# Performance work log

Measured on AMD Instinct MI355X. Metric: run time of the kernel, lower is better.

The kernel has to match this reference:

```python
import jax, jax.numpy as jnp
import numpy as np

LEAKY = 0.1
NSAMPLE = 16


def _gather_group(p, idx):
    # p: [B, N, C], idx: [B, S, K] -> [B, S, K, C]
    return jax.vmap(lambda pb, ib: pb[ib])(p, idx)


def _knn_idx(x, k):
    # x: [B, N, 3]; squared pairwise distances, smallest-k indices
    sq = jnp.sum(x * x, axis=-1)  # [B, N]
    d = sq[:, :, None] + sq[:, None, :] - 2.0 * jnp.einsum('bnc,bmc->bnm', x, x)
    _, idx = jax.lax.top_k(-d, k)  # [B, N, K]
    return idx


def setup_inputs() -> dict:
    key = jax.random.key(0)
    k1, k2, k3, k4, k5 = jax.random.split(key, 5)
    B, N, D = 4, 8192, 32
    m0, m1, m2 = 32, 32, 64
    xyz = jax.random.normal(k1, (B, 3, N), dtype=jnp.float32)
    points = jax.random.normal(k2, (B, D, N), dtype=jnp.float32)
    # Conv2d 1x1 weights (kernel dims squeezed): [out, in]
    W0 = jax.random.normal(k3, (m0, D + 3), dtype=jnp.float32) * (1.0 / np.sqrt(D + 3))
    W1 = jax.random.normal(k4, (m1, m0), dtype=jnp.float32) * (1.0 / np.sqrt(m0))
    W2 = jax.random.normal(k5, (m2, m1), dtype=jnp.float32) * (1.0 / np.sqrt(m1))
    return {'xyz': xyz, 'points': points, 'W0': W0, 'W1': W1, 'W2': W2}


def reference(xyz, points, W0, W1, W2):
    lrelu = lambda x: jax.nn.leaky_relu(x, LEAKY)
    xyz_t = jnp.swapaxes(xyz, 1, 2)  # [B, N, 3]
    # pre-transform point features with feature part of first conv weight
    feat = jnp.einsum('oc,bcn->bno', W0[:, 3:], points)  # [B, N, m0]
    idx = _knn_idx(xyz_t, NSAMPLE)  # [B, N, K]
    grouped_xyz = _gather_group(xyz_t, idx)              # [B, N, K, 3]
    grouped_norm = grouped_xyz - xyz_t[:, :, None, :]    # relative coords
    grouped_feat = _gather_group(feat, idx)              # [B, N, K, m0]
    # first conv: xyz-part applied to relative coords + already-transformed feats
    x = jnp.einsum('oc,bnkc->bonk', W0[:, :3], grouped_norm) \
        + jnp.transpose(grouped_feat, (0, 3, 1, 2))      # [B, m0, N, K]
    x = lrelu(x)
    x = lrelu(jnp.einsum('oc,bcnk->bonk', W1, x))        # [B, m1, N, K]
    x = lrelu(jnp.einsum('oc,bcnk->bonk', W2, x))        # [B, m2, N, K]
    return jnp.max(x, axis=-1)                           # [B, m2, N]
```

## Files before the change

kernel.cpp:

```cpp
#include <hip/hip_runtime.h>

#define NP   8192
#define BB   4
#define DIN  32
#define M0   32
#define M1   32
#define M2   64
#define CAP  80
#define CSTR 81
#define KQ   32

typedef float f32x2 __attribute__((ext_vector_type(2)));
typedef float f32x4 __attribute__((ext_vector_type(4)));
typedef short bf16x8 __attribute__((ext_vector_type(8)));

__device__ __forceinline__ float lrelu(float x) { return fmaxf(x, 0.1f * x); }
__device__ __forceinline__ unsigned umin_(unsigned a, unsigned b) { return a < b ? a : b; }
__device__ __forceinline__ unsigned umax_(unsigned a, unsigned b) { return a > b ? a : b; }

__device__ __forceinline__ unsigned fkey(float f) {
    unsigned b = __float_as_uint(f);
    return (b & 0x80000000u) ? ~b : (b | 0x80000000u);
}
__device__ __forceinline__ float funkey(unsigned k) {
    unsigned b = (k & 0x80000000u) ? (k & 0x7fffffffu) : ~k;
    return __uint_as_float(b);
}

__device__ __forceinline__ unsigned bf16rn(float f) {
    unsigned u = __float_as_uint(f);
    unsigned r = (u >> 16) & 1u;
    return (u + 0x7fffu + r) >> 16;
}

__device__ __forceinline__ f32x2 pk_fma(f32x2 a, f32x2 b, f32x2 c) {
    f32x2 d;
    asm("v_pk_fma_f32 %0, %1, %2, %3" : "=v"(d) : "v"(a), "s"(b), "v"(c));
    return d;
}

__device__ __forceinline__ void split_pack2(float f0, float f1, unsigned& hp, unsigned& lp) {
    unsigned u0 = __float_as_uint(f0), u1 = __float_as_uint(f1);
    unsigned h0 = u0 & 0xffff0000u, h1 = u1 & 0xffff0000u;
    hp = (u0 >> 16) | h1;
    float r0 = f0 - __uint_as_float(h0);
    float r1 = f1 - __uint_as_float(h1);
    lp = (__float_as_uint(r0) >> 16) | (__float_as_uint(r1) & 0xffff0000u);
}

__device__ __forceinline__ void wfrag(const float* wrow, bf16x8& h, bf16x8& lo) {
    float4 a = *(const float4*)(wrow);
    float4 b = *(const float4*)(wrow + 4);
    unsigned* hv = (unsigned*)&h;
    unsigned* lv = (unsigned*)&lo;
    split_pack2(a.x, a.y, hv[0], lv[0]);
    split_pack2(a.z, a.w, hv[1], lv[1]);
    split_pack2(b.x, b.y, hv[2], lv[2]);
    split_pack2(b.z, b.w, hv[3], lv[3]);
}

__device__ __forceinline__ f32x4 mfma16(bf16x8 a, bf16x8 b, f32x4 c) {
    return __builtin_amdgcn_mfma_f32_16x16x32_bf16(a, b, c, 0, 0, 0);
}

__global__ __launch_bounds__(256) void prep_kernel(
    const float* __restrict__ xyz, const float* __restrict__ points,
    const float* __restrict__ W0, const float* __restrict__ W1,
    const float* __restrict__ W2, float4* __restrict__ pts4,
    float4* __restrict__ ptsS, unsigned* __restrict__ featb,
    uint4* __restrict__ w1f, uint4* __restrict__ w2f)
{
    const int tid  = threadIdx.x;
    const int w    = __builtin_amdgcn_readfirstlane(tid >> 6);
    const int lane = tid & 63;
    const int t    = blockIdx.x * 64 + lane;
    const int b    = t >> 13;
    const int n    = t & (NP - 1);

    if (w == 0) {
        const float* xb = xyz + (size_t)b * 3 * NP;
        float x = xb[n], y = xb[NP + n], z = xb[2 * NP + n];
        float s = x * x + y * y + z * z;
        pts4[t] = make_float4(x, y, z, s);
        ptsS[t] = make_float4(-2.f * x, -2.f * y, -2.f * z, s);
    }

    const float* pb = points + (size_t)b * DIN * NP + n;
    float p[DIN];
#pragma unroll
    for (int c = 0; c < DIN; ++c) p[c] = pb[c * NP];

    uint4 outv;
    unsigned* ov = (unsigned*)&outv;
#pragma unroll
    for (int r = 0; r < 4; ++r) {
        int oe = w * 8 + 2 * r;
        float a0 = 0.f, a1 = 0.f;
#pragma unroll
        for (int c = 0; c < DIN; ++c) {
            a0 = fmaf(W0[oe * 35 + 3 + c], p[c], a0);
            a1 = fmaf(W0[(oe + 1) * 35 + 3 + c], p[c], a1);
        }
        ov[r] = bf16rn(a0) | (bf16rn(a1) << 16);
    }
    *(uint4*)(featb + (size_t)t * 16 + w * 4) = outv;

    if (blockIdx.x == 0 && tid < 64) {
        const int qq = tid & 15, gg = tid >> 4;
        bf16x8 h, lo;
#pragma unroll
        for (int r = 0; r < 2; ++r) {
            wfrag(W1 + (16 * r + qq) * 32 + gg * 8, h, lo);
            w1f[(r * 64 + tid) * 2 + 0] = *(uint4*)&h;
            w1f[(r * 64 + tid) * 2 + 1] = *(uint4*)&lo;
        }
#pragma unroll
        for (int rr = 0; rr < 4; ++rr) {
            wfrag(W2 + (16 * rr + qq) * 32 + gg * 8, h, lo);
            w2f[(rr * 64 + tid) * 2 + 0] = *(uint4*)&h;
            w2f[(rr * 64 + tid) * 2 + 1] = *(uint4*)&lo;
        }
    }
}

__global__ __launch_bounds__(512, 8) void knn_kernel(const float4* __restrict__ pts4,
                                                     const float4* __restrict__ ptsS,
                                                     int* __restrict__ idxout)
{
    __shared__ unsigned skey[KQ * 65];
    __shared__ float    sT[KQ];
    __shared__ int      scnt[KQ];
    __shared__ float    cand_t[KQ * CSTR];
    __shared__ int      cand_i[KQ * CSTR];

    const int tid  = threadIdx.x;
    const int w    = __builtin_amdgcn_readfirstlane(tid >> 6);
    const int lane = tid & 63;
    const int blk  = blockIdx.x;
    const int b    = blk >> 8;
    const int n0   = (blk & 255) << 5;
    const int bn0  = b * NP;
    const float4* P  = pts4 + bn0;
    const float4* S  = ptsS + bn0;
    const float4* Pq = P + n0;

    for (int i = tid; i < KQ * 65; i += 512) skey[i] = 0xFFFFFFFFu;
    if (tid < KQ) scnt[tid] = 0;
    __syncthreads();

    const int base = w * 1024;

#pragma unroll 1
    for (int sg = 0; sg < 2; ++sg) {
        const int sb = base + sg * 512;
        f32x2 sx[4], sy[4], sz[4], sw2[4];
#pragma unroll
        for (int jp = 0; jp < 4; ++jp) {
            float4 a = S[sb + (2 * jp) * 64 + lane];
            float4 c = S[sb + (2 * jp + 1) * 64 + lane];
            sx[jp].x = a.x;  sx[jp].y = c.x;
            sy[jp].x = a.y;  sy[jp].y = c.y;
            sz[jp].x = a.z;  sz[jp].y = c.z;
            sw2[jp].x = a.w; sw2[jp].y = c.w;
        }
#pragma unroll 1
        for (int qc = 0; qc < 4; ++qc) {
            float4 qv[8];
#pragma unroll
            for (int i = 0; i < 8; ++i) qv[i] = Pq[qc * 8 + i];
#pragma unroll
            for (int i = 0; i < 8; ++i) {
                f32x2 qx, qy, qz;
                qx.x = qv[i].x; qx.y = qv[i].x;
                qy.x = qv[i].y; qy.y = qv[i].y;
                qz.x = qv[i].z; qz.y = qv[i].z;
                f32x2 t0 = pk_fma(sz[0], qz, sw2[0]);
                f32x2 t1 = pk_fma(sz[1], qz, sw2[1]);
                f32x2 t2 = pk_fma(sz[2], qz, sw2[2]);
                f32x2 t3 = pk_fma(sz[3], qz, sw2[3]);
                t0 = pk_fma(sy[0], qy, t0);  t1 = pk_fma(sy[1], qy, t1);
                t2 = pk_fma(sy[2], qy, t2);  t3 = pk_fma(sy[3], qy, t3);
                t0 = pk_fma(sx[0], qx, t0);  t1 = pk_fma(sx[1], qx, t1);
                t2 = pk_fma(sx[2], qx, t2);  t3 = pk_fma(sx[3], qx, t3);
                float a  = fminf(fminf(t0.x, t0.y), t1.x);
                float b2 = fminf(fminf(t1.y, t2.x), t2.y);
                float c2 = fminf(fminf(t3.x, t3.y), a);
                float mn = fminf(b2, c2);
                atomicMin(&skey[(qc * 8 + i) * 65 + lane], fkey(mn));
            }
        }
    }
    __syncthreads();

    if (tid < KQ) {
        unsigned t16[16];
#pragma unroll
        for (int i = 0; i < 16; ++i) t16[i] = 0xFFFFFFFFu;
        for (int c = 0; c < 64; ++c) {
            unsigned d = skey[tid * 65 + c];
            if (d < t16[15]) {
                t16[15] = d;
#pragma unroll
                for (int i = 15; i > 0; --i) {
                    unsigned a = t16[i - 1], cc = t16[i];
                    t16[i - 1] = umin_(a, cc);
                    t16[i]     = umax_(a, cc);
                }
            }
        }
        sT[tid] = funkey(t16[15]);
    }
    __syncthreads();

#pragma unroll 1
    for (int sg = 0; sg < 2; ++sg) {
        const int sb = base + sg * 512;
        f32x2 sx[4], sy[4], sz[4], sw2[4];
#pragma unroll
        for (int jp = 0; jp < 4; ++jp) {
            float4 a = S[sb + (2 * jp) * 64 + lane];
            float4 c = S[sb + (2 * jp + 1) * 64 + lane];
            sx[jp].x = a.x;  sx[jp].y = c.x;
            sy[jp].x = a.y;  sy[jp].y = c.y;
            sz[jp].x = a.z;  sz[jp].y = c.z;
            sw2[jp].x = a.w; sw2[jp].y = c.w;
        }
#pragma unroll 1
        for (int qc = 0; qc < 4; ++qc) {
            float4 qv[8];
#pragma unroll
            for (int i = 0; i < 8; ++i) qv[i] = Pq[qc * 8 + i];
#pragma unroll
            for (int i = 0; i < 8; ++i) {
                const int q = qc * 8 + i;
                const float T = sT[q];
                f32x2 qx, qy, qz;
                qx.x = qv[i].x; qx.y = qv[i].x;
                qy.x = qv[i].y; qy.y = qv[i].y;
                qz.x = qv[i].z; qz.y = qv[i].z;
#pragma unroll
                for (int jp = 0; jp < 4; ++jp) {
                    f32x2 t = pk_fma(sz[jp], qz, sw2[jp]);
                    t = pk_fma(sy[jp], qy, t);
                    t = pk_fma(sx[jp], qx, t);
                    if (t.x <= T) {
                        int pos = atomicAdd(&scnt[q], 1);
                        if (pos < CAP) {
                            cand_t[q * CSTR + pos] = t.x;
                            cand_i[q * CSTR + pos] = sb + (2 * jp) * 64 + lane;
                        }
                    }
                    if (t.y <= T) {
                        int pos = atomicAdd(&scnt[q], 1);
                        if (pos < CAP) {
                            cand_t[q * CSTR + pos] = t.y;
                            cand_i[q * CSTR + pos] = sb + (2 * jp + 1) * 64 + lane;
                        }
                    }
                }
            }
        }
    }
    __syncthreads();

    if (tid < KQ) {
        int cnt = scnt[tid];
        int* outp = idxout + ((bn0 + n0 + tid) << 4);
        float bd[16]; int bi[16];
#pragma unroll
        for (int i = 0; i < 16; ++i) { bd[i] = 3e38f; bi[i] = 0; }
        if (cnt <= CAP) {
            for (int pos = 0; pos < cnt; ++pos) {
                float d = cand_t[tid * CSTR + pos];
                int   j = cand_i[tid * CSTR + pos];
                if ((d < bd[15]) || (d == bd[15] && j < bi[15])) {
                    bd[15] = d; bi[15] = j;
#pragma unroll
                    for (int i = 15; i > 0; --i) {
                        bool sw = (bd[i] < bd[i - 1]) || (bd[i] == bd[i - 1] && bi[i] < bi[i - 1]);
                        float td = bd[i - 1]; int tj = bi[i - 1];
                        bd[i - 1] = sw ? bd[i] : td;  bi[i - 1] = sw ? bi[i] : tj;
                        bd[i]     = sw ? td : bd[i];  bi[i]     = sw ? tj : bi[i];
                    }
                }
            }
        } else {
            float4 q4 = Pq[tid];
            for (int j = 0; j < NP; ++j) {
                float4 s = S[j];
                float d = fmaf(q4.x, s.x, fmaf(q4.y, s.y, fmaf(q4.z, s.z, s.w)));
                if ((d < bd[15]) || (d == bd[15] && j < bi[15])) {
                    bd[15] = d; bi[15] = j;
#pragma unroll
                    for (int i = 15; i > 0; --i) {
                        bool sw = (bd[i] < bd[i - 1]) || (bd[i] == bd[i - 1] && bi[i] < bi[i - 1]);
                        float td = bd[i - 1]; int tj = bi[i - 1];
                        bd[i - 1] = sw ? bd[i] : td;  bi[i - 1] = sw ? bi[i] : tj;
                        bd[i]     = sw ? td : bd[i];  bi[i]     = sw ? tj : bi[i];
                    }
                }
            }
        }
#pragma unroll
        for (int i = 0; i < 16; ++i) outp[i] = bi[i];
    }
}

__global__ __launch_bounds__(256, 4) void conv_kernel(
    const float4* __restrict__ pts4, const unsigned* __restrict__ featb,
    const int* __restrict__ idx, const float* __restrict__ W0,
    const uint4* __restrict__ w1f, const uint4* __restrict__ w2f,
    float* __restrict__ out)
{
    __shared__ __align__(16) unsigned short sh_hi[4][4][64][8];
    __shared__ __align__(16) unsigned short sh_lo[4][4][64][8];
    __shared__ float so[M2][17];

    const int tid = threadIdx.x;
    const int w   = __builtin_amdgcn_readfirstlane(tid >> 6);
    const int l   = tid & 63;
    const int g   = l >> 4;
    const int q   = l & 15;
    const int k   = tid & 15;
    const int nl  = tid >> 4;
    const int blk = blockIdx.x;
    const int b   = blk >> 9;
    const int n0  = (blk & 511) << 4;
    const int n   = n0 + nl;
    const int bn  = b * NP + n;
    const int j   = idx[(bn << 4) + k];
    const int bj  = b * NP + j;

    const float4 pc = pts4[bn];
    const float4 pj = pts4[bj];
    const float rx = pj.x - pc.x, ry = pj.y - pc.y, rz = pj.z - pc.z;

    const uint4* fj = (const uint4*)(featb + (size_t)bj * 16);

#pragma unroll
    for (int gg = 0; gg < 4; ++gg) {
        uint4 u = fj[gg];
        const unsigned* uv = (const unsigned*)&u;
        uint4 hv, lv;
        unsigned* hp = (unsigned*)&hv;
        unsigned* lp = (unsigned*)&lv;
#pragma unroll
        for (int r = 0; r < 4; ++r) {
            int o = gg * 8 + 2 * r;
            float fe  = __uint_as_float(uv[r] << 16);
            float fo_ = __uint_as_float(uv[r] & 0xffff0000u);
            float e0 = lrelu(fmaf(W0[o * 35], rx, fmaf(W0[o * 35 + 1], ry, fmaf(W0[o * 35 + 2], rz, fe))));
            float e1 = lrelu(fmaf(W0[(o + 1) * 35], rx, fmaf(W0[(o + 1) * 35 + 1], ry, fmaf(W0[(o + 1) * 35 + 2], rz, fo_))));
            split_pack2(e0, e1, hp[r], lp[r]);
        }
        *(uint4*)&sh_hi[w][gg][l][0] = hv;
        *(uint4*)&sh_lo[w][gg][l][0] = lv;
    }

    bf16x8 b1h[4], b1l[4];
#pragma unroll
    for (int t = 0; t < 4; ++t) {
        b1h[t] = *(const bf16x8*)&sh_hi[w][g][16 * t + q][0];
        b1l[t] = *(const bf16x8*)&sh_lo[w][g][16 * t + q][0];
    }
    const f32x4 zz = {0.f, 0.f, 0.f, 0.f};
#pragma unroll
    for (int r = 0; r < 2; ++r) {
        bf16x8 wh = *(const bf16x8*)&w1f[(r * 64 + l) * 2 + 0];
        bf16x8 wl = *(const bf16x8*)&w1f[(r * 64 + l) * 2 + 1];
#pragma unroll
        for (int t = 0; t < 4; ++t) {
            f32x4 a = mfma16(wl, b1h[t], zz);
            a = mfma16(wh, b1l[t], a);
            a = mfma16(wh, b1h[t], a);
            float v0 = lrelu(a[0]);
            float v1 = lrelu(a[1]);
            float v2 = lrelu(a[2]);
            float v3 = lrelu(a[3]);
            uint2 hv, lv;
            split_pack2(v0, v1, hv.x, lv.x);
            split_pack2(v2, v3, hv.y, lv.y);
            const int kg = 2 * r + (g >> 1);
            const int ko = 4 * (g & 1);
            *(uint2*)&sh_hi[w][kg][16 * t + q][ko] = hv;
            *(uint2*)&sh_lo[w][kg][16 * t + q][ko] = lv;
        }
    }

    bf16x8 b2h[4], b2l[4];
#pragma unroll
    for (int t = 0; t < 4; ++t) {
        b2h[t] = *(const bf16x8*)&sh_hi[w][g][16 * t + q][0];
        b2l[t] = *(const bf16x8*)&sh_lo[w][g][16 * t + q][0];
    }
#pragma unroll
    for (int rr = 0; rr < 4; ++rr) {
        bf16x8 wh = *(const bf16x8*)&w2f[(rr * 64 + l) * 2 + 0];
        bf16x8 wl = *(const bf16x8*)&w2f[(rr * 64 + l) * 2 + 1];
#pragma unroll
        for (int t = 0; t < 4; ++t) {
            f32x4 a = mfma16(b2h[t], wl, zz);
            a = mfma16(b2l[t], wh, a);
            a = mfma16(b2h[t], wh, a);
            float m = fmaxf(fmaxf(a[0], a[1]), fmaxf(a[2], a[3]));
            m = fmaxf(m, __int_as_float(__builtin_amdgcn_ds_swizzle(__float_as_int(m), 0x401F)));
            m = fmaxf(m, __shfl_xor(m, 32));
            if (g == 0) so[16 * rr + q][w * 4 + t] = lrelu(m);
        }
    }
    __syncthreads();
    {
        int o = tid >> 2;
        int col = (tid & 3) << 2;
        float4 v = make_float4(so[o][col], so[o][col + 1], so[o][col + 2], so[o][col + 3]);
        *(float4*)(out + ((size_t)(b * M2 + o)) * NP + n0 + col) = v;
    }
}

extern "C" void kernel_launch(void* const* d_in, const int* in_sizes, int n_in,
                              void* d_out, int out_size, void* d_ws, size_t ws_size,
                              hipStream_t stream)
{
    const float* xyz    = (const float*)d_in[0];
    const float* points = (const float*)d_in[1];
    const float* W0     = (const float*)d_in[2];
    const float* W1     = (const float*)d_in[3];
    const float* W2     = (const float*)d_in[4];
    float* out = (float*)d_out;

    char* ws = (char*)d_ws;
    float4*   pts4  = (float4*)ws;
    float4*   ptsS  = (float4*)(ws + 0x080000);
    unsigned* featb = (unsigned*)(ws + 0x100000);
    int*      idx   = (int*)(ws + 0x300000);
    uint4*    w1f   = (uint4*)(ws + 0x500000);
    uint4*    w2f   = (uint4*)(ws + 0x502000);

    prep_kernel<<<BB * NP / 64, 256,  0, stream>>>(xyz, points, W0, W1, W2, pts4, ptsS, featb, w1f, w2f);
    knn_kernel <<<BB * NP / KQ, 512,  0, stream>>>(pts4, ptsS, idx);
    conv_kernel<<<BB * NP / 16, 256,  0, stream>>>(pts4, featb, idx, W0, w1f, w2f, out);
}
```

Baseline: 185.4 us.

## Parallelize kNN threshold and final top-16 selection with wave-wide bitonic sorts

Replaces the serial per-thread insertion sorts, run by only 32 threads, with wave-level bitonic sorts using shuffles, so each wave handles 4 queries across all 64 lanes. Both the threshold selection and the final top-16 candidate selection change this way, and overflow candidates past 64 are merged by ballot-rank insertion. The brute-force fallback now runs on a single lane. The conv kernel also aliases its output staging buffer onto sh_lo to cut LDS use, which needs an extra barrier.

```diff
diff --git a/kernel.cpp b/kernel.cpp
--- a/kernel.cpp
+++ b/kernel.cpp
@@ -192,23 +192,22 @@
     }
     __syncthreads();
 
-    if (tid < KQ) {
-        unsigned t16[16];
-#pragma unroll
-        for (int i = 0; i < 16; ++i) t16[i] = 0xFFFFFFFFu;
-        for (int c = 0; c < 64; ++c) {
-            unsigned d = skey[tid * 65 + c];
-            if (d < t16[15]) {
-                t16[15] = d;
-#pragma unroll
-                for (int i = 15; i > 0; --i) {
-                    unsigned a = t16[i - 1], cc = t16[i];
-                    t16[i - 1] = umin_(a, cc);
-                    t16[i]     = umax_(a, cc);
-                }
-            }
-        }
-        sT[tid] = funkey(t16[15]);
+#pragma unroll 1
+    for (int qi = 0; qi < 4; ++qi) {
+        const int q = w * 4 + qi;
+        unsigned v = skey[q * 65 + lane];
+#pragma unroll
+        for (int k = 2; k <= 64; k <<= 1) {
+#pragma unroll
+            for (int j = k >> 1; j >= 1; j >>= 1) {
+                unsigned o = __shfl_xor(v, j);
+                bool lower = (lane & j) == 0;
+                bool up    = (lane & k) == 0;
+                unsigned mn = umin_(v, o), mx = umax_(v, o);
+                v = (lower == up) ? mn : mx;
+            }
+        }
+        if (lane == 15) sT[q] = funkey(v);
     }
     __syncthreads();
 
@@ -263,16 +262,50 @@
     }
     __syncthreads();
 
-    if (tid < KQ) {
-        int cnt = scnt[tid];
-        int* outp = idxout + ((bn0 + n0 + tid) << 4);
-        float bd[16]; int bi[16];
-#pragma unroll
-        for (int i = 0; i < 16; ++i) { bd[i] = 3e38f; bi[i] = 0; }
+#pragma unroll 1
+    for (int qi = 0; qi < 4; ++qi) {
+        const int q = w * 4 + qi;
+        const int cnt = scnt[q];
+        int* outp = idxout + ((bn0 + n0 + q) << 4);
         if (cnt <= CAP) {
-            for (int pos = 0; pos < cnt; ++pos) {
-                float d = cand_t[tid * CSTR + pos];
-                int   j = cand_i[tid * CSTR + pos];
+            unsigned kh = 0xFFFFFFFFu, kl = 0xFFFFFFFFu;
+            if (lane < cnt) {
+                kh = fkey(cand_t[q * CSTR + lane]);
+                kl = (unsigned)cand_i[q * CSTR + lane];
+            }
+#pragma unroll
+            for (int k = 2; k <= 64; k <<= 1) {
+#pragma unroll
+                for (int j = k >> 1; j >= 1; j >>= 1) {
+                    unsigned oh = __shfl_xor(kh, j);
+                    unsigned ol = __shfl_xor(kl, j);
+                    bool lower = (lane & j) == 0;
+                    bool up    = (lane & k) == 0;
+                    bool lt    = (kh < oh) || (kh == oh && kl < ol);
+                    bool keep  = ((lower == up) == lt);
+                    kh = keep ? kh : oh;
+                    kl = keep ? kl : ol;
+                }
+            }
+            for (int e = 64; e < cnt; ++e) {
+                unsigned eh = fkey(cand_t[q * CSTR + e]);
+                unsigned el = (unsigned)cand_i[q * CSTR + e];
+                unsigned long long less = __ballot((kh < eh) || (kh == eh && kl < el));
+                int r = (int)__popcll(less);
+                unsigned ph = __shfl_up(kh, 1);
+                unsigned pl = __shfl_up(kl, 1);
+                if (lane == r)      { kh = eh; kl = el; }
+                else if (lane > r)  { kh = ph; kl = pl; }
+            }
+            if (lane < 16) outp[lane] = (int)kl;
+        } else if (lane == 0) {
+            float bd[16]; int bi[16];
+#pragma unroll
+            for (int i = 0; i < 16; ++i) { bd[i] = 3e38f; bi[i] = 0; }
+            float4 q4 = Pq[q];
+            for (int j = 0; j < NP; ++j) {
+                float4 s = S[j];
+                float d = fmaf(q4.x, s.x, fmaf(q4.y, s.y, fmaf(q4.z, s.z, s.w)));
                 if ((d < bd[15]) || (d == bd[15] && j < bi[15])) {
                     bd[15] = d; bi[15] = j;
 #pragma unroll
@@ -284,25 +317,9 @@
                     }
                 }
             }
-        } else {
-            float4 q4 = Pq[tid];
-            for (int j = 0; j < NP; ++j) {
-                float4 s = S[j];
-                float d = fmaf(q4.x, s.x, fmaf(q4.y, s.y, fmaf(q4.z, s.z, s.w)));
-                if ((d < bd[15]) || (d == bd[15] && j < bi[15])) {
-                    bd[15] = d; bi[15] = j;
-#pragma unroll
-                    for (int i = 15; i > 0; --i) {
-                        bool sw = (bd[i] < bd[i - 1]) || (bd[i] == bd[i - 1] && bi[i] < bi[i - 1]);
-                        float td = bd[i - 1]; int tj = bi[i - 1];
-                        bd[i - 1] = sw ? bd[i] : td;  bi[i - 1] = sw ? bi[i] : tj;
-                        bd[i]     = sw ? td : bd[i];  bi[i]     = sw ? tj : bi[i];
-                    }
-                }
-            }
-        }
-#pragma unroll
-        for (int i = 0; i < 16; ++i) outp[i] = bi[i];
+#pragma unroll
+            for (int i = 0; i < 16; ++i) outp[i] = bi[i];
+        }
     }
 }
 
@@ -314,7 +331,7 @@
 {
     __shared__ __align__(16) unsigned short sh_hi[4][4][64][8];
     __shared__ __align__(16) unsigned short sh_lo[4][4][64][8];
-    __shared__ float so[M2][17];
+    float* soF = (float*)&sh_lo[0][0][0][0];
 
     const int tid = threadIdx.x;
     const int w   = __builtin_amdgcn_readfirstlane(tid >> 6);
@@ -393,6 +410,8 @@
         b2h[t] = *(const bf16x8*)&sh_hi[w][g][16 * t + q][0];
         b2l[t] = *(const bf16x8*)&sh_lo[w][g][16 * t + q][0];
     }
+    __syncthreads();
+
 #pragma unroll
     for (int rr = 0; rr < 4; ++rr) {
         bf16x8 wh = *(const bf16x8*)&w2f[(rr * 64 + l) * 2 + 0];
@@ -405,14 +424,15 @@
             float m = fmaxf(fmaxf(a[0], a[1]), fmaxf(a[2], a[3]));
             m = fmaxf(m, __int_as_float(__builtin_amdgcn_ds_swizzle(__float_as_int(m), 0x401F)));
             m = fmaxf(m, __shfl_xor(m, 32));
-            if (g == 0) so[16 * rr + q][w * 4 + t] = lrelu(m);
+            if (g == 0) soF[(16 * rr + q) * 17 + w * 4 + t] = lrelu(m);
         }
     }
     __syncthreads();
     {
         int o = tid >> 2;
         int col = (tid & 3) << 2;
-        float4 v = make_float4(so[o][col], so[o][col + 1], so[o][col + 2], so[o][col + 3]);
+        float4 v = make_float4(soF[o * 17 + col], soF[o * 17 + col + 1],
+                               soF[o * 17 + col + 2], soF[o * 17 + col + 3]);
         *(float4*)(out + ((size_t)(b * M2 + o)) * NP + n0 + col) = v;
     }
 }
```

After: 172.7 us (median of 2 runs). -6.8%, faster.
